# Kernel optimization log

Measured on AMD Instinct MI355X. Metric: run time of the kernel, lower is better.

The kernel has to match this reference:

```python
import jax, jax.numpy as jnp
import numpy as np

D = 2048
N_DRUG, N_PROT = 10000, 20000
E = 100000


def setup_inputs() -> dict:
    key = jax.random.key(0)
    ks = jax.random.split(key, 10)
    return {
        "x_drug": jax.random.normal(ks[0], (N_DRUG, D), dtype=jnp.float32),
        "x_protein": jax.random.normal(ks[1], (N_PROT, D), dtype=jnp.float32),
        "rel_ddi": jax.random.normal(ks[2], (D,), dtype=jnp.float32),
        "rel_dpi": jax.random.normal(ks[3], (D,), dtype=jnp.float32),
        "ddi_src": jax.random.randint(ks[4], (E,), 0, N_DRUG, dtype=jnp.int64 if jax.config.jax_enable_x64 else jnp.int32),
        "ddi_dst": jax.random.randint(ks[5], (E,), 0, N_DRUG, dtype=jnp.int64 if jax.config.jax_enable_x64 else jnp.int32),
        "dpi_src": jax.random.randint(ks[6], (E,), 0, N_DRUG, dtype=jnp.int64 if jax.config.jax_enable_x64 else jnp.int32),
        "dpi_dst": jax.random.randint(ks[7], (E,), 0, N_PROT, dtype=jnp.int64 if jax.config.jax_enable_x64 else jnp.int32),
        "ppi_src": jax.random.randint(ks[8], (E,), 0, N_PROT, dtype=jnp.int64 if jax.config.jax_enable_x64 else jnp.int32),
        "ppi_dst": jax.random.randint(ks[9], (E,), 0, N_PROT, dtype=jnp.int64 if jax.config.jax_enable_x64 else jnp.int32),
    }


def _edge_score(x_src, x_dst, src, dst, rel):
    # gather [E, D] head/tail, DistMult-style multiply-reduce, clamp to [0, 1]
    head = x_src[src]
    tail = x_dst[dst]
    score = jnp.sum(head * rel * tail, axis=-1)
    return jnp.clip(score, 0.0, 1.0)


def reference(x_drug, x_protein, rel_ddi, rel_dpi,
              ddi_src, ddi_dst, dpi_src, dpi_dst, ppi_src, ppi_dst):
    score_ddi = _edge_score(x_drug, x_drug, ddi_src, ddi_dst, rel_ddi)
    score_dpi = _edge_score(x_drug, x_protein, dpi_src, dpi_dst, rel_dpi)
    # NOTE: original module (faithfully) applies the DPI relation to PPI edges
    score_ppi = _edge_score(x_protein, x_protein, ppi_src, ppi_dst, rel_dpi)
    return (score_ddi, score_dpi, score_ppi)
```

## Files before the change

### kernel.cpp

```cpp
#include <hip/hip_runtime.h>

#define D4 512
#define K_EDGES 16


__global__ void zero_ints(int* __restrict__ p, int n) {
    int i = blockIdx.x * blockDim.x + threadIdx.x;
    if (i < n) p[i] = 0;
}

__global__ void hist3(const int* __restrict__ s0, const int* __restrict__ s1,
                      const int* __restrict__ s2, int E,
                      int* __restrict__ cnt, int nd) {
    int i = blockIdx.x * blockDim.x + threadIdx.x;
    const int total = 3 * E;
    for (; i < total; i += gridDim.x * blockDim.x) {
        if (i < E)           atomicAdd(&cnt[s0[i]], 1);
        else if (i < 2 * E)  atomicAdd(&cnt[nd + s1[i - E]], 1);
        else                 atomicAdd(&cnt[2 * nd + s2[i - 2 * E]], 1);
    }
}

__global__ void scan3(const int* __restrict__ cnt, int* __restrict__ base,
                      int nd, int np) {
    __shared__ int part[1024];
    const int b = blockIdx.x;
    const int off = (b == 0) ? 0 : (b == 1) ? nd : 2 * nd;
    const int N = (b == 2) ? np : nd;
    const int t = threadIdx.x;
    const int C = (N + blockDim.x - 1) / blockDim.x;
    const int lo = t * C, hi = min(lo + C, N);
    int s = 0;
    for (int i = lo; i < hi; ++i) s += cnt[off + i];
    part[t] = s;
    __syncthreads();
    if (t == 0) {
        int run = 0;
        for (int i = 0; i < (int)blockDim.x; ++i) { int tmp = part[i]; part[i] = run; run += tmp; }
    }
    __syncthreads();
    int run = part[t];
    for (int i = lo; i < hi; ++i) { base[off + i] = run; run += cnt[off + i]; }
}

__global__ void scatter3(const int* __restrict__ s0, const int* __restrict__ s1,
                         const int* __restrict__ s2, int E,
                         int* __restrict__ base, int nd, int* __restrict__ sorted) {
    int i = blockIdx.x * blockDim.x + threadIdx.x;
    const int total = 3 * E;
    for (; i < total; i += gridDim.x * blockDim.x) {
        if (i < E)          { int p = atomicAdd(&base[s0[i]], 1);           sorted[p] = i; }
        else if (i < 2 * E) { int k = i - E;     int p = atomicAdd(&base[nd + s1[k]], 1);     sorted[E + p] = k; }
        else                { int k = i - 2 * E; int p = atomicAdd(&base[2 * nd + s2[k]], 1); sorted[2 * E + p] = k; }
    }
}

__global__ __launch_bounds__(256) void score_sorted(
    const float4* __restrict__ xdrug, const float4* __restrict__ xprot,
    const float4* __restrict__ rddi,  const float4* __restrict__ rdpi,
    const int* __restrict__ ddi_src, const int* __restrict__ ddi_dst,
    const int* __restrict__ dpi_src, const int* __restrict__ dpi_dst,
    const int* __restrict__ ppi_src, const int* __restrict__ ppi_dst,
    const int* __restrict__ sorted, float* __restrict__ out, int E)
{
    const int lane = threadIdx.x & 63;
    const int wpb = blockDim.x >> 6;
    int wid = blockIdx.x * wpb + (threadIdx.x >> 6);
    const int nw = gridDim.x * wpb;
    const int cpr = (E + K_EDGES - 1) / K_EDGES;
    const int total_chunks = 3 * cpr;

    for (int c = wid; c < total_chunks; c += nw) {
        const int r = c / cpr;
        const int ci = c - r * cpr;
        const int e_lo = ci * K_EDGES;
        const int e_hi = min(e_lo + K_EDGES, E);

        const float4 *xs, *xd, *rel;
        const int *srcA, *dstA, *sl;
        float* o;
        if (r == 0)      { xs = xdrug; xd = xdrug; rel = rddi; srcA = ddi_src; dstA = ddi_dst; sl = sorted;         o = out; }
        else if (r == 1) { xs = xdrug; xd = xprot; rel = rdpi; srcA = dpi_src; dstA = dpi_dst; sl = sorted + E;     o = out + E; }
        else             { xs = xprot; xd = xprot; rel = rdpi; srcA = ppi_src; dstA = ppi_dst; sl = sorted + 2 * E; o = out + 2 * E; }

        float4 rr[8];
#pragma unroll
        for (int j = 0; j < 8; ++j) rr[j] = rel[j * 64 + lane];

        int cur_src = -1;
        float4 hr[8];
        for (int i = e_lo; i < e_hi; ++i) {
            const int e = sl[i];
            const int s = srcA[e];
            if (s != cur_src) {
                cur_src = s;
                const float4* __restrict__ hp = xs + (size_t)s * D4;
#pragma unroll
                for (int j = 0; j < 8; ++j) {
                    float4 h = hp[j * 64 + lane];
                    hr[j].x = h.x * rr[j].x;
                    hr[j].y = h.y * rr[j].y;
                    hr[j].z = h.z * rr[j].z;
                    hr[j].w = h.w * rr[j].w;
                }
            }
            const int d = dstA[e];
            const float4* __restrict__ tp = xd + (size_t)d * D4;
            float acc = 0.f;
#pragma unroll
            for (int j = 0; j < 8; ++j) {
                float4 t = tp[j * 64 + lane];
                acc = fmaf(hr[j].x, t.x, acc);
                acc = fmaf(hr[j].y, t.y, acc);
                acc = fmaf(hr[j].z, t.z, acc);
                acc = fmaf(hr[j].w, t.w, acc);
            }
#pragma unroll
            for (int off = 32; off; off >>= 1) acc += __shfl_down(acc, off, 64);
            if (lane == 0) o[e] = fminf(fmaxf(acc, 0.f), 1.f);
        }
    }
}

__global__ __launch_bounds__(256) void edge_score_all(
    const float4* __restrict__ xdrug, const float4* __restrict__ xprot,
    const float4* __restrict__ rddi,  const float4* __restrict__ rdpi,
    const int* __restrict__ ddi_src, const int* __restrict__ ddi_dst,
    const int* __restrict__ dpi_src, const int* __restrict__ dpi_dst,
    const int* __restrict__ ppi_src, const int* __restrict__ ppi_dst,
    float* __restrict__ out, int E)
{
    __shared__ float4 srel[2][D4];
    for (int i = threadIdx.x; i < D4; i += blockDim.x) {
        srel[0][i] = rddi[i];
        srel[1][i] = rdpi[i];
    }
    __syncthreads();
    const int lane = threadIdx.x & 63;
    const int wpb = blockDim.x >> 6;
    int wid = blockIdx.x * wpb + (threadIdx.x >> 6);
    const int nw = gridDim.x * wpb;
    const int total = 3 * E;
    for (int e = wid; e < total; e += nw) {
        const float4 *hp, *tp;
        int sel;
        if (e < E)          { hp = xdrug + (size_t)ddi_src[e] * D4; tp = xdrug + (size_t)ddi_dst[e] * D4; sel = 0; }
        else if (e < 2 * E) { int k = e - E;     hp = xdrug + (size_t)dpi_src[k] * D4; tp = xprot + (size_t)dpi_dst[k] * D4; sel = 1; }
        else                { int k = e - 2 * E; hp = xprot + (size_t)ppi_src[k] * D4; tp = xprot + (size_t)ppi_dst[k] * D4; sel = 1; }
        float acc = 0.f;
#pragma unroll
        for (int j = 0; j < 8; ++j) {
            const int idx = j * 64 + lane;
            float4 h = hp[idx], t = tp[idx], r = srel[sel][idx];
            acc = fmaf(h.x * r.x, t.x, acc);
            acc = fmaf(h.y * r.y, t.y, acc);
            acc = fmaf(h.z * r.z, t.z, acc);
            acc = fmaf(h.w * r.w, t.w, acc);
        }
#pragma unroll
        for (int off = 32; off; off >>= 1) acc += __shfl_down(acc, off, 64);
        if (lane == 0) out[e] = fminf(fmaxf(acc, 0.f), 1.f);
    }
}

extern "C" void kernel_launch(void* const* d_in, const int* in_sizes, int n_in,
                              void* d_out, int out_size, void* d_ws, size_t ws_size,
                              hipStream_t stream) {
    const float* x_drug    = (const float*)d_in[0];
    const float* x_protein = (const float*)d_in[1];
    const float* rel_ddi   = (const float*)d_in[2];
    const float* rel_dpi   = (const float*)d_in[3];
    const int* ddi_src = (const int*)d_in[4];
    const int* ddi_dst = (const int*)d_in[5];
    const int* dpi_src = (const int*)d_in[6];
    const int* dpi_dst = (const int*)d_in[7];
    const int* ppi_src = (const int*)d_in[8];
    const int* ppi_dst = (const int*)d_in[9];

    const int D  = in_sizes[2];
    const int nd = in_sizes[0] / D;
    const int np = in_sizes[1] / D;
    const int E  = in_sizes[4];
    float* out = (float*)d_out;

    const int CB = 2 * nd + np;
    const size_t need = (size_t)(2 * CB + 3 * E) * sizeof(int);

    if (ws_size < need) {
        edge_score_all<<<2048, 256, 0, stream>>>(
            (const float4*)x_drug, (const float4*)x_protein,
            (const float4*)rel_ddi, (const float4*)rel_dpi,
            ddi_src, ddi_dst, dpi_src, dpi_dst, ppi_src, ppi_dst, out, E);
        return;
    }

    int* cnt    = (int*)d_ws;
    int* base   = cnt + CB;
    int* sorted = base + CB;

    zero_ints<<<(CB + 255) / 256, 256, 0, stream>>>(cnt, CB);
    hist3<<<1024, 256, 0, stream>>>(ddi_src, dpi_src, ppi_src, E, cnt, nd);
    scan3<<<3, 1024, 0, stream>>>(cnt, base, nd, np);
    scatter3<<<1024, 256, 0, stream>>>(ddi_src, dpi_src, ppi_src, E, base, nd, sorted);

    const int cpr = (E + K_EDGES - 1) / K_EDGES;
    const int total_chunks = 3 * cpr;
    const int waves_per_block = 4;
    const int blocks = (total_chunks + waves_per_block - 1) / waves_per_block;

    score_sorted<<<blocks, 256, 0, stream>>>(
        (const float4*)x_drug, (const float4*)x_protein,
        (const float4*)rel_ddi, (const float4*)rel_dpi,
        ddi_src, ddi_dst, dpi_src, dpi_dst, ppi_src, ppi_dst,
        sorted, out, E);
}
```

Measured before the change: 713.8 us.

## Replace serial scan with wave-atomic allocation, pack src/dst, prefetch tails, dynamic chunk queue

Replaces the three-block serial prefix scan with a per-wave shuffle scan whose bucket bases come from atomic cursors. This gives a grouping by source that is not globally ordered but stays contiguous per source. The scatter now also writes packed (src<<16|dst) keys, so the scoring kernel loads indices coalesced per chunk and broadcasts them with shuffles. The scoring kernel double-buffers tail-row loads across consecutive edges, doubles the chunk size, and uses a persistent grid with an atomic work queue. Risks are higher register pressure from three float4[8] arrays under a four-waves occupancy bound, and 16-bit packing that only holds for node counts below 65536.

```diff
diff --git a/kernel.cpp b/kernel.cpp
--- a/kernel.cpp
+++ b/kernel.cpp
@@ -1,7 +1,7 @@
 #include <hip/hip_runtime.h>
 
 #define D4 512
-#define K_EDGES 16
+#define K_EDGES 32
 
 
 __global__ void zero_ints(int* __restrict__ p, int n) {
@@ -11,114 +11,172 @@
 
 __global__ void hist3(const int* __restrict__ s0, const int* __restrict__ s1,
                       const int* __restrict__ s2, int E,
-                      int* __restrict__ cnt, int nd) {
+                      int* __restrict__ cnt, int O1, int O2) {
     int i = blockIdx.x * blockDim.x + threadIdx.x;
     const int total = 3 * E;
     for (; i < total; i += gridDim.x * blockDim.x) {
         if (i < E)           atomicAdd(&cnt[s0[i]], 1);
-        else if (i < 2 * E)  atomicAdd(&cnt[nd + s1[i - E]], 1);
-        else                 atomicAdd(&cnt[2 * nd + s2[i - 2 * E]], 1);
-    }
-}
-
-__global__ void scan3(const int* __restrict__ cnt, int* __restrict__ base,
-                      int nd, int np) {
-    __shared__ int part[1024];
-    const int b = blockIdx.x;
-    const int off = (b == 0) ? 0 : (b == 1) ? nd : 2 * nd;
-    const int N = (b == 2) ? np : nd;
-    const int t = threadIdx.x;
-    const int C = (N + blockDim.x - 1) / blockDim.x;
-    const int lo = t * C, hi = min(lo + C, N);
-    int s = 0;
-    for (int i = lo; i < hi; ++i) s += cnt[off + i];
-    part[t] = s;
-    __syncthreads();
-    if (t == 0) {
-        int run = 0;
-        for (int i = 0; i < (int)blockDim.x; ++i) { int tmp = part[i]; part[i] = run; run += tmp; }
-    }
-    __syncthreads();
-    int run = part[t];
-    for (int i = lo; i < hi; ++i) { base[off + i] = run; run += cnt[off + i]; }
-}
-
-__global__ void scatter3(const int* __restrict__ s0, const int* __restrict__ s1,
-                         const int* __restrict__ s2, int E,
-                         int* __restrict__ base, int nd, int* __restrict__ sorted) {
+        else if (i < 2 * E)  atomicAdd(&cnt[O1 + s1[i - E]], 1);
+        else                 atomicAdd(&cnt[O2 + s2[i - 2 * E]], 1);
+    }
+}
+
+__global__ void alloc3(const int* __restrict__ cnt, int* __restrict__ base,
+                       int* __restrict__ cursors, int O1, int O2, int CBp) {
+    int i = blockIdx.x * blockDim.x + threadIdx.x;
+    if (i >= CBp) return;
+    const int lane = threadIdx.x & 63;
+    const int rel = (i >= O2) ? 2 : (i >= O1) ? 1 : 0;
+    int c = cnt[i];
+    int x = c;
+#pragma unroll
+    for (int d = 1; d < 64; d <<= 1) {
+        int y = __shfl_up(x, d, 64);
+        if (lane >= d) x += y;
+    }
+    int tot = __shfl(x, 63);
+    int wb = 0;
+    if (lane == 63) wb = atomicAdd(&cursors[rel], tot);
+    wb = __shfl(wb, 63);
+    base[i] = wb + x - c;
+}
+
+__global__ void scatter3(const int* __restrict__ s0, const int* __restrict__ d0_,
+                         const int* __restrict__ s1, const int* __restrict__ d1_,
+                         const int* __restrict__ s2, const int* __restrict__ d2_,
+                         int E, int* __restrict__ base, int O1, int O2,
+                         int* __restrict__ sorted, int* __restrict__ sd) {
     int i = blockIdx.x * blockDim.x + threadIdx.x;
     const int total = 3 * E;
     for (; i < total; i += gridDim.x * blockDim.x) {
-        if (i < E)          { int p = atomicAdd(&base[s0[i]], 1);           sorted[p] = i; }
-        else if (i < 2 * E) { int k = i - E;     int p = atomicAdd(&base[nd + s1[k]], 1);     sorted[E + p] = k; }
-        else                { int k = i - 2 * E; int p = atomicAdd(&base[2 * nd + s2[k]], 1); sorted[2 * E + p] = k; }
-    }
-}
-
-__global__ __launch_bounds__(256) void score_sorted(
+        if (i < E) {
+            int s = s0[i], d = d0_[i];
+            int p = atomicAdd(&base[s], 1);
+            sorted[p] = i; sd[p] = (s << 16) | d;
+        } else if (i < 2 * E) {
+            int k = i - E; int s = s1[k], d = d1_[k];
+            int p = atomicAdd(&base[O1 + s], 1);
+            sorted[E + p] = k; sd[E + p] = (s << 16) | d;
+        } else {
+            int k = i - 2 * E; int s = s2[k], d = d2_[k];
+            int p = atomicAdd(&base[O2 + s], 1);
+            sorted[2 * E + p] = k; sd[2 * E + p] = (s << 16) | d;
+        }
+    }
+}
+
+__global__ __launch_bounds__(256, 4) void score_sorted(
     const float4* __restrict__ xdrug, const float4* __restrict__ xprot,
     const float4* __restrict__ rddi,  const float4* __restrict__ rdpi,
-    const int* __restrict__ ddi_src, const int* __restrict__ ddi_dst,
-    const int* __restrict__ dpi_src, const int* __restrict__ dpi_dst,
-    const int* __restrict__ ppi_src, const int* __restrict__ ppi_dst,
-    const int* __restrict__ sorted, float* __restrict__ out, int E)
+    const int* __restrict__ sorted, const int* __restrict__ sd,
+    int* __restrict__ queue, float* __restrict__ out, int E)
 {
     const int lane = threadIdx.x & 63;
     const int wpb = blockDim.x >> 6;
-    int wid = blockIdx.x * wpb + (threadIdx.x >> 6);
+    const int wid = blockIdx.x * wpb + (threadIdx.x >> 6);
     const int nw = gridDim.x * wpb;
     const int cpr = (E + K_EDGES - 1) / K_EDGES;
     const int total_chunks = 3 * cpr;
 
-    for (int c = wid; c < total_chunks; c += nw) {
-        const int r = c / cpr;
+    int c = wid;
+    while (c < total_chunks) {
+        const int r = (c >= 2 * cpr) ? 2 : (c >= cpr) ? 1 : 0;
         const int ci = c - r * cpr;
         const int e_lo = ci * K_EDGES;
-        const int e_hi = min(e_lo + K_EDGES, E);
+        const int n = min(K_EDGES, E - e_lo);
 
         const float4 *xs, *xd, *rel;
-        const int *srcA, *dstA, *sl;
-        float* o;
-        if (r == 0)      { xs = xdrug; xd = xdrug; rel = rddi; srcA = ddi_src; dstA = ddi_dst; sl = sorted;         o = out; }
-        else if (r == 1) { xs = xdrug; xd = xprot; rel = rdpi; srcA = dpi_src; dstA = dpi_dst; sl = sorted + E;     o = out + E; }
-        else             { xs = xprot; xd = xprot; rel = rdpi; srcA = ppi_src; dstA = ppi_dst; sl = sorted + 2 * E; o = out + 2 * E; }
-
-        float4 rr[8];
-#pragma unroll
-        for (int j = 0; j < 8; ++j) rr[j] = rel[j * 64 + lane];
-
-        int cur_src = -1;
-        float4 hr[8];
-        for (int i = e_lo; i < e_hi; ++i) {
-            const int e = sl[i];
-            const int s = srcA[e];
-            if (s != cur_src) {
-                cur_src = s;
-                const float4* __restrict__ hp = xs + (size_t)s * D4;
+        if (r == 0)      { xs = xdrug; xd = xdrug; rel = rddi; }
+        else if (r == 1) { xs = xdrug; xd = xprot; rel = rdpi; }
+        else             { xs = xprot; xd = xprot; rel = rdpi; }
+        const int* sl  = sorted + (size_t)r * E + e_lo;
+        const int* sdl = sd     + (size_t)r * E + e_lo;
+        float* o = out + (size_t)r * E;
+
+        int eL = 0, sdL = 0;
+        if (lane < n) { eL = sl[lane]; sdL = sdl[lane]; }
+
+        float4 hr[8], tA[8], tB[8];
+        int cur = -1;
+
+        {
+            int sd0 = __shfl(sdL, 0);
+            const float4* tp = xd + (size_t)(sd0 & 0xffff) * D4;
+#pragma unroll
+            for (int j = 0; j < 8; ++j) tA[j] = tp[j * 64 + lane];
+        }
+
+        for (int i = 0; i < n; i += 2) {
+            if (i + 1 < n) {
+                int sdn = __shfl(sdL, i + 1);
+                const float4* tq = xd + (size_t)(sdn & 0xffff) * D4;
+#pragma unroll
+                for (int j = 0; j < 8; ++j) tB[j] = tq[j * 64 + lane];
+            }
+            {
+                int sdi = __shfl(sdL, i);
+                int s = sdi >> 16;
+                if (s != cur) {
+                    cur = s;
+                    const float4* hp = xs + (size_t)s * D4;
+#pragma unroll
+                    for (int j = 0; j < 8; ++j) {
+                        float4 h = hp[j * 64 + lane], rv = rel[j * 64 + lane];
+                        hr[j].x = h.x * rv.x; hr[j].y = h.y * rv.y;
+                        hr[j].z = h.z * rv.z; hr[j].w = h.w * rv.w;
+                    }
+                }
+                float acc = 0.f;
 #pragma unroll
                 for (int j = 0; j < 8; ++j) {
-                    float4 h = hp[j * 64 + lane];
-                    hr[j].x = h.x * rr[j].x;
-                    hr[j].y = h.y * rr[j].y;
-                    hr[j].z = h.z * rr[j].z;
-                    hr[j].w = h.w * rr[j].w;
-                }
-            }
-            const int d = dstA[e];
-            const float4* __restrict__ tp = xd + (size_t)d * D4;
-            float acc = 0.f;
-#pragma unroll
-            for (int j = 0; j < 8; ++j) {
-                float4 t = tp[j * 64 + lane];
-                acc = fmaf(hr[j].x, t.x, acc);
-                acc = fmaf(hr[j].y, t.y, acc);
-                acc = fmaf(hr[j].z, t.z, acc);
-                acc = fmaf(hr[j].w, t.w, acc);
-            }
-#pragma unroll
-            for (int off = 32; off; off >>= 1) acc += __shfl_down(acc, off, 64);
-            if (lane == 0) o[e] = fminf(fmaxf(acc, 0.f), 1.f);
-        }
+                    acc = fmaf(hr[j].x, tA[j].x, acc);
+                    acc = fmaf(hr[j].y, tA[j].y, acc);
+                    acc = fmaf(hr[j].z, tA[j].z, acc);
+                    acc = fmaf(hr[j].w, tA[j].w, acc);
+                }
+#pragma unroll
+                for (int off = 32; off; off >>= 1) acc += __shfl_down(acc, off, 64);
+                int e = __shfl(eL, i);
+                if (lane == 0) o[e] = fminf(fmaxf(acc, 0.f), 1.f);
+            }
+            if (i + 1 >= n) break;
+            if (i + 2 < n) {
+                int sdn = __shfl(sdL, i + 2);
+                const float4* tq = xd + (size_t)(sdn & 0xffff) * D4;
+#pragma unroll
+                for (int j = 0; j < 8; ++j) tA[j] = tq[j * 64 + lane];
+            }
+            {
+                int sdi = __shfl(sdL, i + 1);
+                int s = sdi >> 16;
+                if (s != cur) {
+                    cur = s;
+                    const float4* hp = xs + (size_t)s * D4;
+#pragma unroll
+                    for (int j = 0; j < 8; ++j) {
+                        float4 h = hp[j * 64 + lane], rv = rel[j * 64 + lane];
+                        hr[j].x = h.x * rv.x; hr[j].y = h.y * rv.y;
+                        hr[j].z = h.z * rv.z; hr[j].w = h.w * rv.w;
+                    }
+                }
+                float acc = 0.f;
+#pragma unroll
+                for (int j = 0; j < 8; ++j) {
+                    acc = fmaf(hr[j].x, tB[j].x, acc);
+                    acc = fmaf(hr[j].y, tB[j].y, acc);
+                    acc = fmaf(hr[j].z, tB[j].z, acc);
+                    acc = fmaf(hr[j].w, tB[j].w, acc);
+                }
+#pragma unroll
+                for (int off = 32; off; off >>= 1) acc += __shfl_down(acc, off, 64);
+                int e = __shfl(eL, i + 1);
+                if (lane == 0) o[e] = fminf(fmaxf(acc, 0.f), 1.f);
+            }
+        }
+
+        int nc = 0;
+        if (lane == 0) nc = atomicAdd(queue, 1);
+        c = nw + __shfl(nc, 0);
     }
 }
 
@@ -151,11 +209,11 @@
 #pragma unroll
         for (int j = 0; j < 8; ++j) {
             const int idx = j * 64 + lane;
-            float4 h = hp[idx], t = tp[idx], r = srel[sel][idx];
-            acc = fmaf(h.x * r.x, t.x, acc);
-            acc = fmaf(h.y * r.y, t.y, acc);
-            acc = fmaf(h.z * r.z, t.z, acc);
-            acc = fmaf(h.w * r.w, t.w, acc);
+            float4 h = hp[idx], t = tp[idx], rr = srel[sel][idx];
+            acc = fmaf(h.x * rr.x, t.x, acc);
+            acc = fmaf(h.y * rr.y, t.y, acc);
+            acc = fmaf(h.z * rr.z, t.z, acc);
+            acc = fmaf(h.w * rr.w, t.w, acc);
         }
 #pragma unroll
         for (int off = 32; off; off >>= 1) acc += __shfl_down(acc, off, 64);
@@ -183,8 +241,13 @@
     const int E  = in_sizes[4];
     float* out = (float*)d_out;
 
-    const int CB = 2 * nd + np;
-    const size_t need = (size_t)(2 * CB + 3 * E) * sizeof(int);
+    const int ndp = ((nd + 63) / 64) * 64;
+    const int npp = ((np + 63) / 64) * 64;
+    const int O1  = ndp;
+    const int O2  = ndp + ndp;
+    const int CBp = O2 + npp;
+
+    const size_t need = (size_t)(2 * CBp + 8 + 6 * E) * sizeof(int);
 
     if (ws_size < need) {
         edge_score_all<<<2048, 256, 0, stream>>>(
@@ -195,22 +258,19 @@
     }
 
     int* cnt    = (int*)d_ws;
-    int* base   = cnt + CB;
-    int* sorted = base + CB;
-
-    zero_ints<<<(CB + 255) / 256, 256, 0, stream>>>(cnt, CB);
-    hist3<<<1024, 256, 0, stream>>>(ddi_src, dpi_src, ppi_src, E, cnt, nd);
-    scan3<<<3, 1024, 0, stream>>>(cnt, base, nd, np);
-    scatter3<<<1024, 256, 0, stream>>>(ddi_src, dpi_src, ppi_src, E, base, nd, sorted);
-
-    const int cpr = (E + K_EDGES - 1) / K_EDGES;
-    const int total_chunks = 3 * cpr;
-    const int waves_per_block = 4;
-    const int blocks = (total_chunks + waves_per_block - 1) / waves_per_block;
-
-    score_sorted<<<blocks, 256, 0, stream>>>(
+    int* aux    = cnt + CBp;
+    int* base   = aux + 8;
+    int* sorted = base + CBp;
+    int* sd     = sorted + 3 * E;
+
+    zero_ints<<<(CBp + 8 + 255) / 256, 256, 0, stream>>>(cnt, CBp + 8);
+    hist3<<<1024, 256, 0, stream>>>(ddi_src, dpi_src, ppi_src, E, cnt, O1, O2);
+    alloc3<<<(CBp + 255) / 256, 256, 0, stream>>>(cnt, base, aux, O1, O2, CBp);
+    scatter3<<<1024, 256, 0, stream>>>(ddi_src, ddi_dst, dpi_src, dpi_dst,
+                                       ppi_src, ppi_dst, E, base, O1, O2, sorted, sd);
+
+    score_sorted<<<1024, 256, 0, stream>>>(
         (const float4*)x_drug, (const float4*)x_protein,
         (const float4*)rel_ddi, (const float4*)rel_dpi,
-        ddi_src, ddi_dst, dpi_src, dpi_dst, ppi_src, ppi_dst,
-        sorted, out, E);
-}
+        sorted, sd, aux + 3, out, E);
+}
```

Result: no change. 708.6 us (-0.7%).
